# Kernel tuning notes

Hardware: AMD Instinct MI355X
Metric: run time of the kernel (lower is better)

Reference implementation:

```python
import jax, jax.numpy as jnp
import numpy as np

MARGIN = 0.3


def setup_inputs() -> dict:
    key = jax.random.key(0)
    k1, k2 = jax.random.split(key)
    B, D, N_IDS = 8192, 256, 512
    emb = jax.random.normal(k1, (B, D), dtype=jnp.float32)
    emb = emb / jnp.linalg.norm(emb, axis=1, keepdims=True)  # L2-normalized as docstring states
    labels = jax.random.randint(k2, (B,), 0, N_IDS, dtype=jnp.int64)
    return {"embeddings": emb, "labels": labels}


def reference(embeddings, labels):
    B = embeddings.shape[0]
    # pairwise Euclidean distance via cosine similarity (embeddings are L2-normalized)
    sim = jnp.matmul(embeddings, embeddings.T)              # (B, B)
    dist = jnp.sqrt(jnp.clip(2.0 - 2.0 * sim, 0.0) + 1e-12)
    same = labels[:, None] == labels[None, :]               # (B, B)
    eye = jnp.eye(B, dtype=bool)
    pos_mask = same & ~eye
    neg_mask = ~same
    neg_inf = jnp.asarray(-jnp.inf, dist.dtype)
    pos_inf = jnp.asarray(jnp.inf, dist.dtype)
    dist_ap = jnp.max(jnp.where(pos_mask, dist, neg_inf), axis=1)  # hardest positive per anchor
    dist_an = jnp.min(jnp.where(neg_mask, dist, pos_inf), axis=1)  # hardest negative per anchor
    valid = jnp.any(pos_mask, axis=1) & jnp.any(neg_mask, axis=1)
    # MarginRankingLoss(dist_an, dist_ap, y=1) = mean(relu(dist_ap - dist_an + margin)) over valid anchors
    per = jnp.maximum(dist_ap - dist_an + MARGIN, 0.0)
    per = jnp.where(valid, per, 0.0)
    n_valid = jnp.sum(valid.astype(dist.dtype))
    loss = jnp.where(n_valid > 0, jnp.sum(per) / jnp.maximum(n_valid, 1.0), 0.0)
    return loss
```

## Files before the change

kernel.cpp:

```cpp
#include <hip/hip_runtime.h>
#include <hip/hip_bf16.h>


#define BDIM 8192
#define DDIM 256

typedef short bf16x8 __attribute__((ext_vector_type(8)));
typedef float f32x4  __attribute__((ext_vector_type(4)));
typedef unsigned short u16;

static __device__ __forceinline__ bf16x8 ld_frag(const u16* p) {
    return *reinterpret_cast<const bf16x8*>(p);
}

static __device__ __forceinline__ u16 f2bf(float f) {
    union { float f; unsigned int u; } x; x.f = f;
    unsigned int u = x.u;
    unsigned int r = u + 0x7fffu + ((u >> 16) & 1u);
    return (u16)(r >> 16);
}

static __device__ __forceinline__ void gload_lds16(const u16* g, u16* l) {
    __builtin_amdgcn_global_load_lds(
        (const __attribute__((address_space(1))) unsigned int*)g,
        (__attribute__((address_space(3))) unsigned int*)l, 16, 0, 0);
}

__global__ __launch_bounds__(256) void cvt_init_kernel(const float* __restrict__ in,
                                                       u16* __restrict__ out,
                                                       int* __restrict__ minpos,
                                                       int* __restrict__ maxneg) {
    int i = blockIdx.x * 256 + threadIdx.x;
    const float4 v = reinterpret_cast<const float4*>(in)[i];
    ushort4 o;
    o.x = f2bf(v.x); o.y = f2bf(v.y); o.z = f2bf(v.z); o.w = f2bf(v.w);
    reinterpret_cast<ushort4*>(out)[i] = o;
    if (i < BDIM) {
        minpos[i] = 0x7f800000;
        maxneg[i] = 0;
    }
}

__global__ __launch_bounds__(256, 2) void triplet_main(const u16* __restrict__ Ebf,
                                                       const int* __restrict__ labels,
                                                       int* __restrict__ minpos,
                                                       int* __restrict__ maxneg) {
    __shared__ __align__(16) u16 smem[2][32 * DDIM];

    const int tid  = threadIdx.x;
    const int w    = tid >> 6;
    const int l    = tid & 63;
    const int quad = l >> 4;
    const int r16  = l & 15;

    const int mblk  = blockIdx.x * 256 + w * 64;
    const int nbase = blockIdx.y * 512;

    bf16x8 a[4][8];
#pragma unroll
    for (int ms = 0; ms < 4; ++ms) {
        const u16* ap = Ebf + (size_t)(mblk + ms * 16 + r16) * DDIM + quad * 8;
#pragma unroll
        for (int k = 0; k < 8; ++k) a[ms][k] = ld_frag(ap + k * 32);
    }

    int lab_row[4][4];
#pragma unroll
    for (int ms = 0; ms < 4; ++ms)
#pragma unroll
        for (int r = 0; r < 4; ++r)
            lab_row[ms][r] = labels[mblk + ms * 16 + quad * 4 + r];

    float minp[4][4], maxn[4][4];
#pragma unroll
    for (int ms = 0; ms < 4; ++ms)
#pragma unroll
        for (int r = 0; r < 4; ++r) { minp[ms][r] = __builtin_inff(); maxn[ms][r] = -__builtin_inff(); }

    const int qs = quad ^ (r16 & 3);
    const int s4 = (r16 >> 2) & 1;

#pragma unroll
    for (int it = 0; it < 4; ++it) {
        const int q = it * 256 + tid;
        const int r = q >> 5;
        const int c = (q & 31) ^ (r & 7);
        gload_lds16(Ebf + ((size_t)(nbase + r) << 8) + c * 8,
                    &smem[0][0] + it * 2048 + w * 512);
    }

    for (int nn = 0; nn < 16; ++nn) {
        const int cur = nn & 1;
        const int n0  = nbase + nn * 32;

        __syncthreads();

        if (nn + 1 < 16) {
            const int n1 = n0 + 32;
#pragma unroll
            for (int it = 0; it < 4; ++it) {
                const int q = it * 256 + tid;
                const int r = q >> 5;
                const int c = (q & 31) ^ (r & 7);
                gload_lds16(Ebf + ((size_t)(n1 + r) << 8) + c * 8,
                            &smem[cur ^ 1][0] + it * 2048 + w * 512);
            }
        }

        f32x4 acc[4][2];
#pragma unroll
        for (int ms = 0; ms < 4; ++ms)
#pragma unroll
            for (int nt = 0; nt < 2; ++nt)
                acc[ms][nt] = (f32x4){0.f, 0.f, 0.f, 0.f};

        const u16* bb = &smem[cur][0];
        const u16* bnt[2];
#pragma unroll
        for (int nt = 0; nt < 2; ++nt)
            bnt[nt] = bb + (nt * 16 + r16) * DDIM + qs * 8;

#pragma unroll
        for (int k = 0; k < 8; ++k) {
            const int koff = ((k ^ s4) << 5);
            bf16x8 b[2];
#pragma unroll
            for (int nt = 0; nt < 2; ++nt) b[nt] = ld_frag(bnt[nt] + koff);
#pragma unroll
            for (int ms = 0; ms < 4; ++ms)
#pragma unroll
                for (int nt = 0; nt < 2; ++nt)
                    acc[ms][nt] = __builtin_amdgcn_mfma_f32_16x16x32_bf16(
                        a[ms][k], b[nt], acc[ms][nt], 0, 0, 0);
        }

        int lab_c[2];
#pragma unroll
        for (int nt = 0; nt < 2; ++nt) lab_c[nt] = labels[n0 + nt * 16 + r16];

        const bool diagTile = (n0 < mblk + 64) && (mblk < n0 + 32);
        if (__builtin_expect(diagTile, 0)) {
#pragma unroll
            for (int nt = 0; nt < 2; ++nt) {
                const int colg = n0 + nt * 16 + r16;
#pragma unroll
                for (int ms = 0; ms < 4; ++ms)
#pragma unroll
                    for (int r = 0; r < 4; ++r) {
                        const int rowg = mblk + ms * 16 + quad * 4 + r;
                        const float s = acc[ms][nt][r];
                        const bool same = (lab_c[nt] == lab_row[ms][r]);
                        const bool pos  = same && (colg != rowg);
                        minp[ms][r] = fminf(minp[ms][r], pos  ?  s : __builtin_inff());
                        maxn[ms][r] = fmaxf(maxn[ms][r], same ? -__builtin_inff() : s);
                    }
            }
        } else {
#pragma unroll
            for (int nt = 0; nt < 2; ++nt)
#pragma unroll
                for (int ms = 0; ms < 4; ++ms)
#pragma unroll
                    for (int r = 0; r < 4; ++r) {
                        const float s = acc[ms][nt][r];
                        const bool same = (lab_c[nt] == lab_row[ms][r]);
                        minp[ms][r] = fminf(minp[ms][r], same ?  s : __builtin_inff());
                        maxn[ms][r] = fmaxf(maxn[ms][r], same ? -__builtin_inff() : s);
                    }
        }
    }

#pragma unroll
    for (int mask = 1; mask <= 8; mask <<= 1) {
#pragma unroll
        for (int ms = 0; ms < 4; ++ms)
#pragma unroll
            for (int r = 0; r < 4; ++r) {
                minp[ms][r] = fminf(minp[ms][r], __shfl_xor(minp[ms][r], mask, 64));
                maxn[ms][r] = fmaxf(maxn[ms][r], __shfl_xor(maxn[ms][r], mask, 64));
            }
    }
    if (r16 == 0) {
#pragma unroll
        for (int ms = 0; ms < 4; ++ms)
#pragma unroll
            for (int r = 0; r < 4; ++r) {
                const int rowg = mblk + ms * 16 + quad * 4 + r;
                atomicMin(minpos + rowg, __float_as_int(minp[ms][r] + 2.0f));
                atomicMax(maxneg + rowg, __float_as_int(maxn[ms][r] + 2.0f));
            }
    }
}

__global__ __launch_bounds__(1024) void finalize_kernel(const int* __restrict__ minpos,
                                                        const int* __restrict__ maxneg,
                                                        float* __restrict__ out) {
    __shared__ float ssum[16], scnt[16];
    float sum = 0.f, cnt = 0.f;
#pragma unroll
    for (int it = 0; it < 8; ++it) {
        const int i = it * 1024 + threadIdx.x;
        const float mp = __int_as_float(minpos[i]);
        const float mn = __int_as_float(maxneg[i]);
        if (mp < 1e30f && mn > 0.5f) {
            const float dap = sqrtf(fmaxf(6.0f - 2.0f * mp, 0.0f) + 1e-12f);
            const float dan = sqrtf(fmaxf(6.0f - 2.0f * mn, 0.0f) + 1e-12f);
            sum += fmaxf(dap - dan + 0.3f, 0.0f);
            cnt += 1.0f;
        }
    }
#pragma unroll
    for (int off = 32; off > 0; off >>= 1) {
        sum += __shfl_down(sum, off, 64);
        cnt += __shfl_down(cnt, off, 64);
    }
    const int wid = threadIdx.x >> 6;
    if ((threadIdx.x & 63) == 0) { ssum[wid] = sum; scnt[wid] = cnt; }
    __syncthreads();
    if (threadIdx.x == 0) {
        float S = 0.f, C = 0.f;
#pragma unroll
        for (int i = 0; i < 16; ++i) { S += ssum[i]; C += scnt[i]; }
        out[0] = (C > 0.f) ? (S / C) : 0.f;
    }
}

extern "C" void kernel_launch(void* const* d_in, const int* in_sizes, int n_in,
                              void* d_out, int out_size, void* d_ws, size_t ws_size,
                              hipStream_t stream) {
    const float* emb    = (const float*)d_in[0];
    const int*   labels = (const int*)d_in[1];
    float*       out    = (float*)d_out;

    u16* Ebf    = (u16*)d_ws;
    int* minpos = (int*)((char*)d_ws + (size_t)BDIM * DDIM * 2);
    int* maxneg = minpos + BDIM;

    cvt_init_kernel<<<dim3((BDIM * DDIM / 4) / 256), dim3(256), 0, stream>>>(emb, Ebf, minpos, maxneg);
    triplet_main<<<dim3(BDIM / 256, BDIM / 512), dim3(256), 0, stream>>>(Ebf, labels, minpos, maxneg);
    finalize_kernel<<<dim3(1), dim3(1024), 0, stream>>>(minpos, maxneg, out);
}
```

Before: 105.9 us.

## Triple-buffer LDS tiles with explicit vmcnt waits and cache labels in LDS

The column-tile pipeline goes from double to triple buffering. Loads are issued two tiles ahead, and a manual s_waitcnt vmcnt(4) plus a raw s_barrier replaces __syncthreads, so one tile's loads can stay in flight while the current tile is computed. Column labels are preloaded once into shared memory instead of being read from global memory every iteration, and the MFMA loop is wrapped in s_setprio raises. This costs about 16KB more LDS per block, which may affect occupancy with 2 blocks per CU, and the hand-written waitcnt depends on the compiler's exact load counts.

```diff
diff --git a/kernel.cpp b/kernel.cpp
--- a/kernel.cpp
+++ b/kernel.cpp
@@ -45,7 +45,8 @@
                                                        const int* __restrict__ labels,
                                                        int* __restrict__ minpos,
                                                        int* __restrict__ maxneg) {
-    __shared__ __align__(16) u16 smem[2][32 * DDIM];
+    __shared__ __align__(16) u16 smem[3][32 * DDIM];
+    __shared__ int slab[512];
 
     const int tid  = threadIdx.x;
     const int w    = tid >> 6;
@@ -56,6 +57,9 @@
     const int mblk  = blockIdx.x * 256 + w * 64;
     const int nbase = blockIdx.y * 512;
 
+    slab[tid]       = labels[nbase + tid];
+    slab[256 + tid] = labels[nbase + 256 + tid];
+
     bf16x8 a[4][8];
 #pragma unroll
     for (int ms = 0; ms < 4; ++ms) {
@@ -80,32 +84,38 @@
     const int qs = quad ^ (r16 & 3);
     const int s4 = (r16 >> 2) & 1;
 
-#pragma unroll
-    for (int it = 0; it < 4; ++it) {
-        const int q = it * 256 + tid;
-        const int r = q >> 5;
-        const int c = (q & 31) ^ (r & 7);
-        gload_lds16(Ebf + ((size_t)(nbase + r) << 8) + c * 8,
-                    &smem[0][0] + it * 2048 + w * 512);
-    }
-
+    auto stage = [&](int t, int buf) {
+        const int n1 = nbase + t * 32;
+#pragma unroll
+        for (int it = 0; it < 4; ++it) {
+            const int q = it * 256 + tid;
+            const int r = q >> 5;
+            const int c = (q & 31) ^ (r & 7);
+            gload_lds16(Ebf + ((size_t)(n1 + r) << 8) + c * 8,
+                        &smem[buf][0] + it * 2048 + w * 512);
+        }
+    };
+
+    stage(0, 0);
+    stage(1, 1);
+
+    int cur = 0;
+#pragma unroll 1
     for (int nn = 0; nn < 16; ++nn) {
-        const int cur = nn & 1;
-        const int n0  = nbase + nn * 32;
-
-        __syncthreads();
-
-        if (nn + 1 < 16) {
-            const int n1 = n0 + 32;
-#pragma unroll
-            for (int it = 0; it < 4; ++it) {
-                const int q = it * 256 + tid;
-                const int r = q >> 5;
-                const int c = (q & 31) ^ (r & 7);
-                gload_lds16(Ebf + ((size_t)(n1 + r) << 8) + c * 8,
-                            &smem[cur ^ 1][0] + it * 2048 + w * 512);
-            }
-        }
+        if (nn < 15) asm volatile("s_waitcnt vmcnt(4) lgkmcnt(0)" ::: "memory");
+        else         asm volatile("s_waitcnt vmcnt(0) lgkmcnt(0)" ::: "memory");
+        __builtin_amdgcn_s_barrier();
+        __builtin_amdgcn_sched_barrier(0);
+
+        if (nn + 2 < 16) {
+            const int stg = (cur >= 1) ? cur - 1 : 2;
+            stage(nn + 2, stg);
+        }
+
+        const int n0 = nbase + nn * 32;
+        int lab_c[2];
+        lab_c[0] = slab[nn * 32 + r16];
+        lab_c[1] = slab[nn * 32 + 16 + r16];
 
         f32x4 acc[4][2];
 #pragma unroll
@@ -120,6 +130,7 @@
         for (int nt = 0; nt < 2; ++nt)
             bnt[nt] = bb + (nt * 16 + r16) * DDIM + qs * 8;
 
+        __builtin_amdgcn_s_setprio(1);
 #pragma unroll
         for (int k = 0; k < 8; ++k) {
             const int koff = ((k ^ s4) << 5);
@@ -133,10 +144,7 @@
                     acc[ms][nt] = __builtin_amdgcn_mfma_f32_16x16x32_bf16(
                         a[ms][k], b[nt], acc[ms][nt], 0, 0, 0);
         }
-
-        int lab_c[2];
-#pragma unroll
-        for (int nt = 0; nt < 2; ++nt) lab_c[nt] = labels[n0 + nt * 16 + r16];
+        __builtin_amdgcn_s_setprio(0);
 
         const bool diagTile = (n0 < mblk + 64) && (mblk < n0 + 32);
         if (__builtin_expect(diagTile, 0)) {
@@ -168,6 +176,8 @@
                         maxn[ms][r] = fmaxf(maxn[ms][r], same ? -__builtin_inff() : s);
                     }
         }
+
+        cur = (cur == 2) ? 0 : cur + 1;
     }
 
 #pragma unroll
```

After: 107.1 us. No clear change (+1.2%).
